# Kernel tuning notes

Hardware: AMD Instinct MI355X
Metric: run time of the kernel (lower is better)

Reference implementation:

```python
import jax, jax.numpy as jnp
import numpy as np

B, M = 512, 2048            # batch of src-tgt pairs, sampled walk positions per pair
NUM_KEYS = 1_000_000        # unique (node, time) keys in nodetime2emb map
NUM_NODES = 100_000
LP = 4                      # num_layers + 1 (saw encoding width)
ENC = 32                    # enc_dim
FEAT = 64                   # node feature dim (MergeLayer dim2)
D3, D4 = 64, 1              # MergeLayer hidden / output dims


def setup_inputs() -> dict:
    key = jax.random.key(0)
    ks = jax.random.split(key, 12)
    s = 0.05
    return {
        "pos_table": jax.random.uniform(ks[0], (NUM_KEYS, LP), dtype=jnp.float32),
        "node_feat": jax.random.normal(ks[1], (NUM_NODES, FEAT), dtype=jnp.float32),
        "W1": jax.random.normal(ks[2], (LP, ENC), dtype=jnp.float32) * s,
        "b1": jnp.zeros((ENC,), dtype=jnp.float32),
        "W2": jax.random.normal(ks[3], (ENC, ENC), dtype=jnp.float32) * s,
        "b2": jnp.zeros((ENC,), dtype=jnp.float32),
        "Wm1": jax.random.normal(ks[4], (ENC + FEAT, D3), dtype=jnp.float32) * s,
        "bm1": jnp.zeros((D3,), dtype=jnp.float32),
        "Wm2": jax.random.normal(ks[5], (D3, D4), dtype=jnp.float32) * s,
        "bm2": jnp.zeros((D4,), dtype=jnp.float32),
        "key_idx": jax.random.randint(ks[6], (B, M), 0, NUM_KEYS, dtype=jnp.int32),
        "node_idx": jax.random.randint(ks[7], (B, M), 0, NUM_NODES, dtype=jnp.int32),
    }


def reference(pos_table, node_feat, W1, b1, W2, b2, Wm1, bm1, Wm2, bm2, key_idx, node_idx):
    # PositionEncoder.forward: gather saw encodings by (node, time) key,
    # then trainable_embedding = Linear(LP->ENC) -> ReLU -> Linear(ENC->ENC)
    enc = pos_table[key_idx]                       # [B, M, LP] irregular gather
    pe = jax.nn.relu(enc @ W1 + b1) @ W2 + b2      # [B, M, ENC]
    # gather raw node features for the same walk positions
    feat = node_feat[node_idx]                     # [B, M, FEAT] irregular gather
    # MergeLayer (non_linear=True): concat -> fc1 -> ReLU -> fc2
    x = jnp.concatenate([pe, feat], axis=-1)       # [B, M, ENC+FEAT]
    z = jax.nn.relu(x @ Wm1 + bm1) @ Wm2 + bm2     # [B, M, 1]
    return z
```

## Files before the change

kernel.cpp:

```cpp
#include <hip/hip_runtime.h>


typedef _Float16 half8 __attribute__((ext_vector_type(8)));
typedef float floatx4 __attribute__((ext_vector_type(4)));

#define HSTR 40
#define WSTR 104
#define GRID_MAIN 768

__global__ void feat_to_f16(const float* __restrict__ nf,
                            _Float16* __restrict__ o, int n8) {
    int t = blockIdx.x * 256 + threadIdx.x;
    if (t >= n8) return;
    const float4* p = (const float4*)nf + (size_t)t * 2;
    const float4 a = p[0], b = p[1];
    half8 h;
    h[0] = (_Float16)a.x; h[1] = (_Float16)a.y;
    h[2] = (_Float16)a.z; h[3] = (_Float16)a.w;
    h[4] = (_Float16)b.x; h[5] = (_Float16)b.y;
    h[6] = (_Float16)b.z; h[7] = (_Float16)b.w;
    *((half8*)o + t) = h;
}

__device__ __forceinline__ void load_feat2(const _Float16* __restrict__ feat16,
                                           const float* __restrict__ node_feat,
                                           int use_f16, int nd0, int nd1, int q,
                                           half8 fA[2][2]) {
    if (use_f16) {
        const _Float16* fb0 = feat16 + (size_t)nd0 * 64 + q * 8;
        const _Float16* fb1 = feat16 + (size_t)nd1 * 64 + q * 8;
        fA[0][0] = *(const half8*)(fb0);
        fA[0][1] = *(const half8*)(fb0 + 32);
        fA[1][0] = *(const half8*)(fb1);
        fA[1][1] = *(const half8*)(fb1 + 32);
    } else {
        #pragma unroll
        for (int rr = 0; rr < 2; ++rr) {
            const float* fb = node_feat + (size_t)(rr ? nd1 : nd0) * 64 + q * 8;
            #pragma unroll
            for (int kt = 0; kt < 2; ++kt) {
                const float4 lo = *(const float4*)(fb + kt * 32);
                const float4 hi = *(const float4*)(fb + kt * 32 + 4);
                half8 h;
                h[0] = (_Float16)lo.x; h[1] = (_Float16)lo.y;
                h[2] = (_Float16)lo.z; h[3] = (_Float16)lo.w;
                h[4] = (_Float16)hi.x; h[5] = (_Float16)hi.y;
                h[6] = (_Float16)hi.z; h[7] = (_Float16)hi.w;
                fA[rr][kt] = h;
            }
        }
    }
}

__global__ __launch_bounds__(256, 3) void neurtw_r17(
    const float* __restrict__ pos_table,
    const float* __restrict__ node_feat,
    const float* __restrict__ W1,
    const float* __restrict__ b1,
    const float* __restrict__ W2,
    const float* __restrict__ b2,
    const float* __restrict__ Wm1,
    const float* __restrict__ bm1,
    const float* __restrict__ Wm2,
    const float* __restrict__ bm2,
    const int*   __restrict__ key_idx,
    const int*   __restrict__ node_idx,
    const _Float16* __restrict__ feat16,
    int use_f16,
    float*       __restrict__ out,
    int rows)
{
    __shared__ _Float16 hpe[256 * HSTR];
    __shared__ _Float16 wm1t[64 * WSTR];

    const int tid  = threadIdx.x;
    const int lane = tid & 63;
    const int r0   = (tid >> 6) * 64;
    const int ln   = lane & 15;
    const int q    = lane >> 4;

    #pragma unroll
    for (int i = 0; i < 3; ++i) {
        const int task = i * 256 + tid;
        const int n = task & 63, k8 = task >> 6;
        half8 w;
        #pragma unroll
        for (int kk = 0; kk < 8; ++kk)
            w[kk] = (_Float16)Wm1[(k8 * 8 + kk) * 64 + n];
        *(half8*)(&wm1t[n * WSTR + k8 * 8]) = w;
    }

    half8 b_w2[2];
    #pragma unroll
    for (int ct = 0; ct < 2; ++ct)
        #pragma unroll
        for (int j = 0; j < 8; ++j)
            b_w2[ct][j] = (_Float16)W2[(q * 8 + j) * 32 + ct * 16 + ln];
    float b2v[2];
    b2v[0] = b2[ln]; b2v[1] = b2[16 + ln];
    float bm1v[4], wm2v[4];
    #pragma unroll
    for (int ct = 0; ct < 4; ++ct) {
        bm1v[ct] = bm1[ct * 16 + ln];
        wm2v[ct] = Wm2[ct * 16 + ln];
    }
    const float bm2s = bm2[0];

    __syncthreads();

    int base = blockIdx.x * 256;
    int ndr[4];
    #pragma unroll
    for (int rt = 0; rt < 4; ++rt)
        ndr[rt] = node_idx[base + r0 + rt * 16 + ln];
    int kkc = key_idx[base + tid];
    float4 enc = *(const float4*)(pos_table + (size_t)kkc * 4);
    half8 fA01[2][2];
    load_feat2(feat16, node_feat, use_f16, ndr[0], ndr[1], q, fA01);

    while (base < rows) {
        const int nbase = base + GRID_MAIN * 256;
        const bool more = nbase < rows;

        half8 fA23[2][2];
        load_feat2(feat16, node_feat, use_f16, ndr[2], ndr[3], q, fA23);

        int ndr_n[4];
        int kk_n;
        if (more) {
            #pragma unroll
            for (int rt = 0; rt < 4; ++rt)
                ndr_n[rt] = node_idx[nbase + r0 + rt * 16 + ln];
            kk_n = key_idx[nbase + tid];
        } else {
            #pragma unroll
            for (int rt = 0; rt < 4; ++rt)
                ndr_n[rt] = 0;
            kk_n = 0;
        }

        #pragma unroll
        for (int g = 0; g < 4; ++g) {
            half8 hv;
            #pragma unroll
            for (int j8 = 0; j8 < 8; ++j8) {
                const int j = g * 8 + j8;
                float a = fmaf(enc.w, W1[96 + j],
                          fmaf(enc.z, W1[64 + j],
                          fmaf(enc.y, W1[32 + j],
                          fmaf(enc.x, W1[j], b1[j]))));
                hv[j8] = (_Float16)fmaxf(a, 0.0f);
            }
            *(half8*)(&hpe[tid * HSTR + g * 8]) = hv;
        }
        half8 a_h[4];
        #pragma unroll
        for (int rt = 0; rt < 4; ++rt)
            a_h[rt] = *(const half8*)(&hpe[(r0 + rt * 16 + ln) * HSTR + q * 8]);

        floatx4 pc[4][2];
        #pragma unroll
        for (int rt = 0; rt < 4; ++rt)
            #pragma unroll
            for (int ct = 0; ct < 2; ++ct) {
                floatx4 c = {0.f, 0.f, 0.f, 0.f};
                pc[rt][ct] = __builtin_amdgcn_mfma_f32_16x16x32_f16(
                    a_h[rt], b_w2[ct], c, 0, 0, 0);
            }

        #pragma unroll
        for (int rt = 0; rt < 4; ++rt)
            #pragma unroll
            for (int ct = 0; ct < 2; ++ct)
                #pragma unroll
                for (int r = 0; r < 4; ++r)
                    hpe[(r0 + rt * 16 + q * 4 + r) * HSTR + ct * 16 + ln] =
                        (_Float16)(pc[rt][ct][r] + b2v[ct]);

        float4 enc_n = enc;
        if (more)
            enc_n = *(const float4*)(pos_table + (size_t)kk_n * 4);

        floatx4 acc[4][4];
        #pragma unroll
        for (int ct = 0; ct < 4; ++ct) {
            const float bb = bm1v[ct];
            #pragma unroll
            for (int rt = 0; rt < 4; ++rt)
                acc[rt][ct] = (floatx4){bb, bb, bb, bb};
        }

        {
            half8 a_pe[4];
            #pragma unroll
            for (int rt = 0; rt < 4; ++rt)
                a_pe[rt] = *(const half8*)(&hpe[(r0 + rt * 16 + ln) * HSTR + q * 8]);
            half8 b0[4];
            #pragma unroll
            for (int ct = 0; ct < 4; ++ct)
                b0[ct] = *(const half8*)(&wm1t[(ct * 16 + ln) * WSTR + q * 8]);
            #pragma unroll
            for (int rt = 0; rt < 4; ++rt)
                #pragma unroll
                for (int ct = 0; ct < 4; ++ct)
                    acc[rt][ct] = __builtin_amdgcn_mfma_f32_16x16x32_f16(
                        a_pe[rt], b0[ct], acc[rt][ct], 0, 0, 0);
        }

        #pragma unroll
        for (int kt = 0; kt < 2; ++kt) {
            half8 bk[4];
            #pragma unroll
            for (int ct = 0; ct < 4; ++ct)
                bk[ct] = *(const half8*)(&wm1t[(ct * 16 + ln) * WSTR + 32 + kt * 32 + q * 8]);
            #pragma unroll
            for (int ct = 0; ct < 4; ++ct) {
                acc[0][ct] = __builtin_amdgcn_mfma_f32_16x16x32_f16(
                    fA01[0][kt], bk[ct], acc[0][ct], 0, 0, 0);
                acc[1][ct] = __builtin_amdgcn_mfma_f32_16x16x32_f16(
                    fA01[1][kt], bk[ct], acc[1][ct], 0, 0, 0);
                acc[2][ct] = __builtin_amdgcn_mfma_f32_16x16x32_f16(
                    fA23[0][kt], bk[ct], acc[2][ct], 0, 0, 0);
                acc[3][ct] = __builtin_amdgcn_mfma_f32_16x16x32_f16(
                    fA23[1][kt], bk[ct], acc[3][ct], 0, 0, 0);
            }
        }

        half8 fA01_n[2][2];
        load_feat2(feat16, node_feat, use_f16, ndr_n[0], ndr_n[1], q, fA01_n);

        #pragma unroll
        for (int rt = 0; rt < 4; ++rt) {
            #pragma unroll
            for (int r = 0; r < 4; ++r) {
                float p = 0.0f;
                #pragma unroll
                for (int ct = 0; ct < 4; ++ct)
                    p = fmaf(fmaxf(acc[rt][ct][r], 0.0f), wm2v[ct], p);
                p += __shfl_xor(p, 1);
                p += __shfl_xor(p, 2);
                p += __shfl_xor(p, 4);
                p += __shfl_xor(p, 8);
                if (ln == 0)
                    out[base + r0 + rt * 16 + q * 4 + r] = p + bm2s;
            }
        }

        base = nbase;
        #pragma unroll
        for (int rt = 0; rt < 4; ++rt)
            ndr[rt] = ndr_n[rt];
        kkc = kk_n;
        enc = enc_n;
        #pragma unroll
        for (int rr = 0; rr < 2; ++rr)
            #pragma unroll
            for (int kt = 0; kt < 2; ++kt)
                fA01[rr][kt] = fA01_n[rr][kt];
    }
}

extern "C" void kernel_launch(void* const* d_in, const int* in_sizes, int n_in,
                              void* d_out, int out_size, void* d_ws, size_t ws_size,
                              hipStream_t stream) {
    const float* pos_table = (const float*)d_in[0];
    const float* node_feat = (const float*)d_in[1];
    const float* W1        = (const float*)d_in[2];
    const float* b1        = (const float*)d_in[3];
    const float* W2        = (const float*)d_in[4];
    const float* b2        = (const float*)d_in[5];
    const float* Wm1       = (const float*)d_in[6];
    const float* bm1       = (const float*)d_in[7];
    const float* Wm2       = (const float*)d_in[8];
    const float* bm2       = (const float*)d_in[9];
    const int*   key_idx   = (const int*)d_in[10];
    const int*   node_idx  = (const int*)d_in[11];
    float* out = (float*)d_out;

    const int rows  = in_sizes[10];
    const int nfeat = in_sizes[1];

    _Float16* feat16 = (_Float16*)d_ws;
    const size_t need = (size_t)nfeat * sizeof(_Float16);
    const int use_f16 = (ws_size >= need) ? 1 : 0;

    if (use_f16) {
        const int n8 = nfeat / 8;
        feat_to_f16<<<(n8 + 255) / 256, 256, 0, stream>>>(node_feat, feat16, n8);
    }

    neurtw_r17<<<GRID_MAIN, 256, 0, stream>>>(
        pos_table, node_feat, W1, b1, W2, b2, Wm1, bm1, Wm2, bm2,
        key_idx, node_idx, feat16, use_f16, out, rows);
}
```

Before: 154.2 us.

## Switch to per-wave dynamic work stealing via atomic tile cursor

Replaces the fixed block-strided loop over 256-row chunks with per-wavefront 64-row tiles. Each wave grabs its next tile from a global atomic counter in the workspace, which is reset by a memset before launch. The aim is to balance load across waves whose irregular gathers finish at different times and to remove the block-level tail. In exchange it adds one atomic per tile, an extra memset node, and a prefetch of the next tile that now depends on the atomic result.

```diff
diff --git a/kernel.cpp b/kernel.cpp
--- a/kernel.cpp
+++ b/kernel.cpp
@@ -52,7 +52,7 @@
     }
 }
 
-__global__ __launch_bounds__(256, 3) void neurtw_r17(
+__global__ __launch_bounds__(256, 3) void neurtw_r18(
     const float* __restrict__ pos_table,
     const float* __restrict__ node_feat,
     const float* __restrict__ W1,
@@ -67,6 +67,8 @@
     const int*   __restrict__ node_idx,
     const _Float16* __restrict__ feat16,
     int use_f16,
+    int*         __restrict__ cursor,
+    int use_steal,
     float*       __restrict__ out,
     int rows)
 {
@@ -108,19 +110,42 @@
 
     __syncthreads();
 
-    int base = blockIdx.x * 256;
-    int ndr[4];
-    #pragma unroll
-    for (int rt = 0; rt < 4; ++rt)
-        ndr[rt] = node_idx[base + r0 + rt * 16 + ln];
-    int kkc = key_idx[base + tid];
-    float4 enc = *(const float4*)(pos_table + (size_t)kkc * 4);
+    const int NT = (rows + 63) >> 6;
+    const int wid_g = blockIdx.x * 4 + (tid >> 6);
+
+    int t_cur = wid_g;
+    if (use_steal) {
+        int t0;
+        if (lane == 0) t0 = atomicAdd(cursor, 1);
+        t_cur = __shfl(t0, 0);
+    }
+
+    int ndr[4] = {0, 0, 0, 0};
+    int kkc = 0;
+    float4 enc = {0.f, 0.f, 0.f, 0.f};
     half8 fA01[2][2];
-    load_feat2(feat16, node_feat, use_f16, ndr[0], ndr[1], q, fA01);
-
-    while (base < rows) {
-        const int nbase = base + GRID_MAIN * 256;
-        const bool more = nbase < rows;
+    if (t_cur < NT) {
+        const int rb = t_cur << 6;
+        #pragma unroll
+        for (int rt = 0; rt < 4; ++rt)
+            ndr[rt] = node_idx[rb + rt * 16 + ln];
+        kkc = key_idx[rb + lane];
+        enc = *(const float4*)(pos_table + (size_t)kkc * 4);
+        load_feat2(feat16, node_feat, use_f16, ndr[0], ndr[1], q, fA01);
+    }
+
+    while (t_cur < NT) {
+        const int rb = t_cur << 6;
+
+        int t_next;
+        if (use_steal) {
+            int tn;
+            if (lane == 0) tn = atomicAdd(cursor, 1);
+            t_next = __shfl(tn, 0);
+        } else {
+            t_next = t_cur + GRID_MAIN * 4;
+        }
+        const bool more = t_next < NT;
 
         half8 fA23[2][2];
         load_feat2(feat16, node_feat, use_f16, ndr[2], ndr[3], q, fA23);
@@ -128,10 +153,11 @@
         int ndr_n[4];
         int kk_n;
         if (more) {
-            #pragma unroll
-            for (int rt = 0; rt < 4; ++rt)
-                ndr_n[rt] = node_idx[nbase + r0 + rt * 16 + ln];
-            kk_n = key_idx[nbase + tid];
+            const int rbn = t_next << 6;
+            #pragma unroll
+            for (int rt = 0; rt < 4; ++rt)
+                ndr_n[rt] = node_idx[rbn + rt * 16 + ln];
+            kk_n = key_idx[rbn + lane];
         } else {
             #pragma unroll
             for (int rt = 0; rt < 4; ++rt)
@@ -241,12 +267,13 @@
                 p += __shfl_xor(p, 2);
                 p += __shfl_xor(p, 4);
                 p += __shfl_xor(p, 8);
-                if (ln == 0)
-                    out[base + r0 + rt * 16 + q * 4 + r] = p + bm2s;
-            }
-        }
-
-        base = nbase;
+                const int orow = rb + rt * 16 + q * 4 + r;
+                if (ln == 0 && orow < rows)
+                    out[orow] = p + bm2s;
+            }
+        }
+
+        t_cur = t_next;
         #pragma unroll
         for (int rt = 0; rt < 4; ++rt)
             ndr[rt] = ndr_n[rt];
@@ -280,16 +307,21 @@
     const int rows  = in_sizes[10];
     const int nfeat = in_sizes[1];
 
-    _Float16* feat16 = (_Float16*)d_ws;
-    const size_t need = (size_t)nfeat * sizeof(_Float16);
+    int* cursor = (int*)d_ws;
+    const int use_steal = (ws_size >= 4) ? 1 : 0;
+
+    _Float16* feat16 = (_Float16*)((char*)d_ws + 256);
+    const size_t need = 256 + (size_t)nfeat * sizeof(_Float16);
     const int use_f16 = (ws_size >= need) ? 1 : 0;
 
+    if (use_steal)
+        hipMemsetAsync(cursor, 0, 4, stream);
     if (use_f16) {
         const int n8 = nfeat / 8;
         feat_to_f16<<<(n8 + 255) / 256, 256, 0, stream>>>(node_feat, feat16, n8);
     }
 
-    neurtw_r17<<<GRID_MAIN, 256, 0, stream>>>(
+    neurtw_r18<<<GRID_MAIN, 256, 0, stream>>>(
         pos_table, node_feat, W1, b1, W2, b2, Wm1, bm1, Wm2, bm2,
-        key_idx, node_idx, feat16, use_f16, out, rows);
+        key_idx, node_idx, feat16, use_f16, cursor, use_steal, out, rows);
 }
```

New measurement: 340.3 us. +120.6%, slower.

## Prefetch all four feature row-tiles one iteration ahead and stage outputs in LDS

Applied to the files above, without the earlier changes.

Moves the fA23 feature gather out of the current iteration so both halves are prefetched a full iteration ahead. The merge MFMAs are split into two phases, and each half's next-tile load is issued as soon as its registers are consumed, which reuses the same registers without copies. Per-row outputs are written to shared memory first and then stored to global as one coalesced 64-float write per wave. The aim is to hide gather latency better, at the cost of longer register live ranges and possibly lower occupancy.

```diff
diff --git a/kernel.cpp b/kernel.cpp
--- a/kernel.cpp
+++ b/kernel.cpp
@@ -52,7 +52,7 @@
     }
 }
 
-__global__ __launch_bounds__(256, 3) void neurtw_r17(
+__global__ __launch_bounds__(256, 3) void neurtw_r19(
     const float* __restrict__ pos_table,
     const float* __restrict__ node_feat,
     const float* __restrict__ W1,
@@ -115,15 +115,13 @@
         ndr[rt] = node_idx[base + r0 + rt * 16 + ln];
     int kkc = key_idx[base + tid];
     float4 enc = *(const float4*)(pos_table + (size_t)kkc * 4);
-    half8 fA01[2][2];
+    half8 fA01[2][2], fA23[2][2];
     load_feat2(feat16, node_feat, use_f16, ndr[0], ndr[1], q, fA01);
+    load_feat2(feat16, node_feat, use_f16, ndr[2], ndr[3], q, fA23);
 
     while (base < rows) {
         const int nbase = base + GRID_MAIN * 256;
         const bool more = nbase < rows;
-
-        half8 fA23[2][2];
-        load_feat2(feat16, node_feat, use_f16, ndr[2], ndr[3], q, fA23);
 
         int ndr_n[4];
         int kk_n;
@@ -214,21 +212,30 @@
             for (int ct = 0; ct < 4; ++ct)
                 bk[ct] = *(const half8*)(&wm1t[(ct * 16 + ln) * WSTR + 32 + kt * 32 + q * 8]);
             #pragma unroll
-            for (int ct = 0; ct < 4; ++ct) {
-                acc[0][ct] = __builtin_amdgcn_mfma_f32_16x16x32_f16(
-                    fA01[0][kt], bk[ct], acc[0][ct], 0, 0, 0);
-                acc[1][ct] = __builtin_amdgcn_mfma_f32_16x16x32_f16(
-                    fA01[1][kt], bk[ct], acc[1][ct], 0, 0, 0);
-                acc[2][ct] = __builtin_amdgcn_mfma_f32_16x16x32_f16(
-                    fA23[0][kt], bk[ct], acc[2][ct], 0, 0, 0);
-                acc[3][ct] = __builtin_amdgcn_mfma_f32_16x16x32_f16(
-                    fA23[1][kt], bk[ct], acc[3][ct], 0, 0, 0);
-            }
-        }
-
-        half8 fA01_n[2][2];
-        load_feat2(feat16, node_feat, use_f16, ndr_n[0], ndr_n[1], q, fA01_n);
-
+            for (int rr = 0; rr < 2; ++rr)
+                #pragma unroll
+                for (int ct = 0; ct < 4; ++ct)
+                    acc[rr][ct] = __builtin_amdgcn_mfma_f32_16x16x32_f16(
+                        fA01[rr][kt], bk[ct], acc[rr][ct], 0, 0, 0);
+        }
+        load_feat2(feat16, node_feat, use_f16, ndr_n[0], ndr_n[1], q, fA01);
+
+        #pragma unroll
+        for (int kt = 0; kt < 2; ++kt) {
+            half8 bk[4];
+            #pragma unroll
+            for (int ct = 0; ct < 4; ++ct)
+                bk[ct] = *(const half8*)(&wm1t[(ct * 16 + ln) * WSTR + 32 + kt * 32 + q * 8]);
+            #pragma unroll
+            for (int rr = 0; rr < 2; ++rr)
+                #pragma unroll
+                for (int ct = 0; ct < 4; ++ct)
+                    acc[2 + rr][ct] = __builtin_amdgcn_mfma_f32_16x16x32_f16(
+                        fA23[rr][kt], bk[ct], acc[2 + rr][ct], 0, 0, 0);
+        }
+        load_feat2(feat16, node_feat, use_f16, ndr_n[2], ndr_n[3], q, fA23);
+
+        float* s_out = (float*)&hpe[r0 * HSTR];
         #pragma unroll
         for (int rt = 0; rt < 4; ++rt) {
             #pragma unroll
@@ -242,9 +249,10 @@
                 p += __shfl_xor(p, 4);
                 p += __shfl_xor(p, 8);
                 if (ln == 0)
-                    out[base + r0 + rt * 16 + q * 4 + r] = p + bm2s;
-            }
-        }
+                    s_out[rt * 16 + q * 4 + r] = p + bm2s;
+            }
+        }
+        out[base + r0 + lane] = s_out[lane];
 
         base = nbase;
         #pragma unroll
@@ -252,11 +260,6 @@
             ndr[rt] = ndr_n[rt];
         kkc = kk_n;
         enc = enc_n;
-        #pragma unroll
-        for (int rr = 0; rr < 2; ++rr)
-            #pragma unroll
-            for (int kt = 0; kt < 2; ++kt)
-                fA01[rr][kt] = fA01_n[rr][kt];
     }
 }
 
@@ -289,7 +292,7 @@
         feat_to_f16<<<(n8 + 255) / 256, 256, 0, stream>>>(node_feat, feat16, n8);
     }
 
-    neurtw_r17<<<GRID_MAIN, 256, 0, stream>>>(
+    neurtw_r19<<<GRID_MAIN, 256, 0, stream>>>(
         pos_table, node_feat, W1, b1, W2, b2, Wm1, bm1, Wm2, bm2,
         key_idx, node_idx, feat16, use_f16, out, rows);
 }
```

After: 172.7 us. 1.12x slower.
